# Optimization experiments

Measured on AMD Instinct MI355X. Metric: run time of the kernel, lower is better.

Reference implementation:

```python
import jax, jax.numpy as jnp
import numpy as np

BEV_H, BEV_W, ED, HEADS, HD, LEVELS, POINTS, LAYERS = 200, 200, 128, 8, 16, 4, 8, 2
SPATIAL = [(128, 256), (64, 128), (32, 64), (16, 32)]
NV = sum(h * w for h, w in SPATIAL)
NQ = BEV_H * BEV_W
NCLS = 21


def setup_inputs() -> dict:
    key = jax.random.key(0)
    ks = iter(jax.random.split(key, 48))
    r = lambda shape, s=0.02: jax.random.normal(next(ks), shape, jnp.float32) * s
    inp = dict(
        value=r((1, NV, ED), 1.0),
        bev_queries=r((NQ, ED), 0.02),
        bev_pos=r((NQ, ED), 0.02),
        proj_indices=jax.random.randint(next(ks), (1, BEV_H, BEV_W), 0, 250000),
        Wv=r((LAYERS, ED, ED)), bv=jnp.zeros((LAYERS, ED)),
        Woff=r((LAYERS, ED, HEADS * LEVELS * POINTS * 2), 0.01),
        boff=jnp.zeros((LAYERS, HEADS * LEVELS * POINTS * 2)),
        Wattn=r((LAYERS, ED, HEADS * LEVELS * POINTS), 0.01),
        battn=jnp.zeros((LAYERS, HEADS * LEVELS * POINTS)),
        Wout=r((LAYERS, ED, ED)), bout=jnp.zeros((LAYERS, ED)),
        Wf1=r((LAYERS, ED, ED)), bf1=jnp.zeros((LAYERS, ED)),
        Wf2=r((LAYERS, ED, ED)), bf2=jnp.zeros((LAYERS, ED)),
        ln_g=jnp.ones((LAYERS, 2, ED)), ln_b=jnp.zeros((LAYERS, 2, ED)),
        cw1=r((128, ED, 7, 7), 0.01), g1=jnp.ones(128), b1=jnp.zeros(128),
        cw2=r((64, 128, 3, 3), 0.02), g2=jnp.ones(64), b2=jnp.zeros(64),
        cw3=r((48, 64, 3, 3), 0.02), g3=jnp.ones(48), b3=jnp.zeros(48),
        cw4=r((48, 48, 3, 3), 0.02), g4=jnp.ones(48), b4=jnp.zeros(48),
        objw=r((NCLS, 48, 1, 1), 0.05), objb=jnp.zeros(NCLS),
    )
    return inp


def _ln(x, g, b):
    m = x.mean(-1, keepdims=True)
    v = ((x - m) ** 2).mean(-1, keepdims=True)
    return (x - m) * jax.lax.rsqrt(v + 1e-5) * g + b


def _deform_attn(q, value, Wv, bv, Woff, boff, Wattn, battn, Wout, bout, ref):
    # multi-scale deformable attention (Deformable-DETR / BEVFormer core)
    v = (value[0] @ Wv + bv).reshape(NV, HEADS, HD)
    off = (q @ Woff + boff).reshape(NQ, HEADS, LEVELS, POINTS, 2)
    attn = jax.nn.softmax((q @ Wattn + battn).reshape(NQ, HEADS, LEVELS * POINTS), -1)
    attn = attn.reshape(NQ, HEADS, LEVELS, POINTS)
    out = jnp.zeros((HEADS, NQ, HD), jnp.float32)
    start = 0
    for l, (H, W) in enumerate(SPATIAL):
        vl = v[start:start + H * W].transpose(1, 0, 2)  # [HEADS, H*W, HD]
        start += H * W
        # normalized sampling locations in [0,1]
        loc = ref[:, None, None, :] + off[:, :, l] / jnp.array([W, H], jnp.float32)
        x = loc[..., 0] * W - 0.5  # grid_sample align_corners=False convention
        y = loc[..., 1] * H - 0.5  # [NQ, HEADS, POINTS]
        x0 = jnp.floor(x)
        y0 = jnp.floor(y)
        acc = jnp.zeros((HEADS, NQ, POINTS, HD), jnp.float32)
        for dx, dy in ((0, 0), (1, 0), (0, 1), (1, 1)):
            xc = x0 + dx
            yc = y0 + dy
            wgt = (1.0 - jnp.abs(x - xc)) * (1.0 - jnp.abs(y - yc))
            valid = (xc >= 0) & (xc < W) & (yc >= 0) & (yc < H)
            xi = jnp.clip(xc, 0, W - 1).astype(jnp.int32)
            yi = jnp.clip(yc, 0, H - 1).astype(jnp.int32)
            idx = (yi * W + xi).transpose(1, 0, 2)  # [HEADS, NQ, POINTS]
            g = jax.vmap(lambda vh, ih: vh[ih])(vl, idx)  # [HEADS, NQ, POINTS, HD]
            acc = acc + (wgt * valid).transpose(1, 0, 2)[..., None] * g
        out = out + jnp.einsum('nhp,hnpd->hnd', attn[:, :, l], acc)
    return out.transpose(1, 0, 2).reshape(NQ, ED) @ Wout + bout


def _bev_encoder(bev_queries, bev_pos, value, Wv, bv, Woff, boff, Wattn, battn, Wout, bout, Wf1, bf1, Wf2, bf2, ln_g, ln_b):
    gx = (jnp.arange(BEV_W, dtype=jnp.float32) + 0.5) / BEV_W
    gy = (jnp.arange(BEV_H, dtype=jnp.float32) + 0.5) / BEV_H
    ref = jnp.stack(jnp.meshgrid(gx, gy), -1).reshape(NQ, 2)  # (x, y)
    q = bev_queries
    for i in range(LAYERS):  # operation_order: cross_attn, norm, ffn, norm
        a = _deform_attn(q + bev_pos, value, Wv[i], bv[i], Woff[i], boff[i],
                         Wattn[i], battn[i], Wout[i], bout[i], ref)
        q = _ln(q + a, ln_g[i, 0], ln_b[i, 0])
        h = jax.nn.relu(q @ Wf1[i] + bf1[i]) @ Wf2[i] + bf2[i]
        q = _ln(q + h, ln_g[i, 1], ln_b[i, 1])
    return q


def _conv(x, w, p):
    return jax.lax.conv_general_dilated(x, w, (1, 1), [(p, p), (p, p)],
                                        dimension_numbers=('NCHW', 'OIHW', 'NCHW'))


def _bn_relu(x, g, b):
    m = x.mean((0, 2, 3), keepdims=True)
    v = x.var((0, 2, 3), keepdims=True)
    return jax.nn.relu((x - m) * jax.lax.rsqrt(v + 1e-5) * g[None, :, None, None] + b[None, :, None, None])


def reference(value, bev_queries, bev_pos, proj_indices, Wv, bv, Woff, boff, Wattn, battn, Wout, bout, Wf1, bf1, Wf2, bf2, ln_g, ln_b, cw1, g1, b1, cw2, g2, b2, cw3, g3, b3, cw4, g4, b4, objw, objb):
    observed_masks = proj_indices < jnp.max(proj_indices)  # mask_update
    q = _bev_encoder(bev_queries, bev_pos, value, Wv, bv, Woff, boff, Wattn, battn,
                     Wout, bout, Wf1, bf1, Wf2, bf2, ln_g, ln_b)
    mem = q.reshape(1, BEV_H, BEV_W, ED).transpose(0, 3, 1, 2)  # [1, ED, H, W]
    h = _bn_relu(_conv(mem, cw1, 3), g1, b1)
    h = _bn_relu(_conv(h, cw2, 1), g2, b2)
    h = _bn_relu(_conv(h, cw3, 1), g3, b3)
    h = _bn_relu(_conv(h, cw4, 1), g4, b4)
    semmap = _conv(h, objw, 0) + objb[None, :, None, None]
    return semmap, observed_masks
```

## Files before the change

### kernel.cpp

```cpp
#include <hip/hip_runtime.h>
#include <cstdint>
#include <cstddef>

#define NQ 40000
#define EDIM 128
#define NVAL 43520
#define NCLS 21

typedef unsigned short u16;
typedef unsigned int uint;
typedef short bf16x8 __attribute__((ext_vector_type(8)));
typedef float f32x4 __attribute__((ext_vector_type(4)));

__device__ inline u16 f2b(float f) {
    unsigned u = __float_as_uint(f);
    unsigned r = u + 0x7FFF + ((u >> 16) & 1);
    return (u16)(r >> 16);
}
__device__ inline float b2f(u16 v) {
    unsigned u = ((unsigned)v) << 16;
    return __uint_as_float(u);
}
__device__ inline float blo(uint u) { return __uint_as_float(u << 16); }
__device__ inline float bhi(uint u) { return __uint_as_float(u & 0xFFFF0000u); }

__global__ void reduce_max_int(const int* __restrict__ idx, int* __restrict__ mx) {
    int i = blockIdx.x * 256 + threadIdx.x;
    int v = (i < NQ) ? idx[i] : 0;
    for (int o = 32; o > 0; o >>= 1) v = max(v, __shfl_xor(v, o, 64));
    if ((threadIdx.x & 63) == 0) atomicMax(mx, v);
}

__global__ void write_mask(const int* __restrict__ idx, const int* __restrict__ mx,
                           float* __restrict__ out) {
    int i = blockIdx.x * 256 + threadIdx.x;
    if (i >= NQ) return;
    out[i] = (idx[i] < *mx) ? 1.0f : 0.0f;
}

__global__ void cvt_b_k(const float* __restrict__ src, u16* __restrict__ dst, int n8) {
    int i = blockIdx.x * 256 + threadIdx.x;
    if (i >= n8) return;
    const float4 a = ((const float4*)src)[i * 2];
    const float4 b = ((const float4*)src)[i * 2 + 1];
    u16 o[8] = {f2b(a.x), f2b(a.y), f2b(a.z), f2b(a.w), f2b(b.x), f2b(b.y), f2b(b.z), f2b(b.w)};
    ((uint4*)dst)[i] = *(const uint4*)o;
}

__global__ void add2b_k(const float* __restrict__ a, const float* __restrict__ b,
                        u16* __restrict__ c, int n8) {
    int i = blockIdx.x * 256 + threadIdx.x;
    if (i >= n8) return;
    const float4 a0 = ((const float4*)a)[i * 2], a1 = ((const float4*)a)[i * 2 + 1];
    const float4 b0 = ((const float4*)b)[i * 2], b1 = ((const float4*)b)[i * 2 + 1];
    u16 o[8] = {f2b(a0.x + b0.x), f2b(a0.y + b0.y), f2b(a0.z + b0.z), f2b(a0.w + b0.w),
                f2b(a1.x + b1.x), f2b(a1.y + b1.y), f2b(a1.z + b1.z), f2b(a1.w + b1.w)};
    ((uint4*)c)[i] = *(const uint4*)o;
}

__global__ void pack_enc_k(const float* __restrict__ Wv, const float* __restrict__ Woff,
                           const float* __restrict__ Wattn, const float* __restrict__ Wout,
                           const float* __restrict__ Wf1, const float* __restrict__ Wf2,
                           u16* __restrict__ dst) {
    int i = blockIdx.x * 256 + threadIdx.x;
    if (i >= 327680) return;
    int l = i / 163840, r = i % 163840;
    int k = r / 1280, col = r % 1280;
    const float* src; int N; int n; u16* d;
    u16* base = dst + (size_t)l * 163840;
    if (col < 128)       { src = Wv    + (size_t)l * 16384; N = 128; n = col;        d = base;          }
    else if (col < 640)  { src = Woff  + (size_t)l * 65536; N = 512; n = col - 128;  d = base + 16384;  }
    else if (col < 896)  { src = Wattn + (size_t)l * 32768; N = 256; n = col - 640;  d = base + 81920;  }
    else if (col < 1024) { src = Wout  + (size_t)l * 16384; N = 128; n = col - 896;  d = base + 114688; }
    else if (col < 1152) { src = Wf1   + (size_t)l * 16384; N = 128; n = col - 1024; d = base + 131072; }
    else                 { src = Wf2   + (size_t)l * 16384; N = 128; n = col - 1152; d = base + 147456; }
    d[(size_t)n * 128 + k] = f2b(src[(size_t)k * N + n]);
}

__global__ void pack_bias_k(const float* __restrict__ boff, const float* __restrict__ battn,
                            float* __restrict__ dst) {
    int i = blockIdx.x * 256 + threadIdx.x;
    if (i >= 1536) return;
    int l = i / 768, r = i % 768;
    dst[i] = (r < 512) ? boff[(size_t)l * 512 + r] : battn[(size_t)l * 256 + r - 512];
}

__global__ void pack_cw_k(const float* __restrict__ w, u16* __restrict__ wT,
                          int OC, int IC, int KS, int OCp, int ICp) {
    int i = blockIdx.x * 256 + threadIdx.x;
    int tot = KS * KS * OCp * ICp;
    if (i >= tot) return;
    int ic = i % ICp; int r = i / ICp;
    int oc = r % OCp; int tap = r / OCp;
    int ky = tap / KS, kx = tap % KS;
    float v = 0.f;
    if (oc < OC && ic < IC)
        v = w[(((size_t)oc * IC + ic) * KS + ky) * KS + kx];
    wT[i] = f2b(v);
}

__global__ __launch_bounds__(256) void gemm_mfma_k(
        const u16* __restrict__ A, const u16* __restrict__ BT,
        const float* __restrict__ bias, float* __restrict__ Cf,
        u16* __restrict__ Cb, int N, int relu) {
    __shared__ u16 As[64 * 136];
    __shared__ u16 Bs[64 * 136];
    const int m0 = blockIdx.x * 64, n0 = blockIdx.y * 64;
    const int t = threadIdx.x;
#pragma unroll
    for (int ci = t; ci < 1024; ci += 256) {
        int r = ci >> 4, c = ci & 15;
        *(uint4*)&As[r * 136 + c * 8] = *(const uint4*)&A[(size_t)(m0 + r) * 128 + c * 8];
        *(uint4*)&Bs[r * 136 + c * 8] = *(const uint4*)&BT[(size_t)(n0 + r) * 128 + c * 8];
    }
    __syncthreads();
    const int wave = t >> 6, lane = t & 63;
    const int wm = (wave & 1) * 32, wn = (wave >> 1) * 32;
    const int lr = lane & 15, lk = (lane >> 4) * 8;
    f32x4 acc[2][2] = {};
#pragma unroll
    for (int ks = 0; ks < 4; ks++) {
        bf16x8 a0 = *(const bf16x8*)&As[(wm + lr) * 136 + ks * 32 + lk];
        bf16x8 a1 = *(const bf16x8*)&As[(wm + 16 + lr) * 136 + ks * 32 + lk];
        bf16x8 b0 = *(const bf16x8*)&Bs[(wn + lr) * 136 + ks * 32 + lk];
        bf16x8 b1 = *(const bf16x8*)&Bs[(wn + 16 + lr) * 136 + ks * 32 + lk];
        acc[0][0] = __builtin_amdgcn_mfma_f32_16x16x32_bf16(a0, b0, acc[0][0], 0, 0, 0);
        acc[0][1] = __builtin_amdgcn_mfma_f32_16x16x32_bf16(a0, b1, acc[0][1], 0, 0, 0);
        acc[1][0] = __builtin_amdgcn_mfma_f32_16x16x32_bf16(a1, b0, acc[1][0], 0, 0, 0);
        acc[1][1] = __builtin_amdgcn_mfma_f32_16x16x32_bf16(a1, b1, acc[1][1], 0, 0, 0);
    }
    float bj0 = bias[n0 + wn + lr];
    float bj1 = bias[n0 + wn + 16 + lr];
#pragma unroll
    for (int i = 0; i < 2; i++) {
#pragma unroll
        for (int j = 0; j < 2; j++) {
            float bb = j ? bj1 : bj0;
#pragma unroll
            for (int r = 0; r < 4; r++) {
                int ml = wm + i * 16 + (lane >> 4) * 4 + r;
                int nl = wn + j * 16 + lr;
                float v = acc[i][j][r] + bb;
                if (relu) v = fmaxf(v, 0.f);
                size_t o = (size_t)(m0 + ml) * N + n0 + nl;
                if (Cf) Cf[o] = v;
                if (Cb) Cb[o] = f2b(v);
            }
        }
    }
}

template <int KS, int ICP>
__global__ __launch_bounds__(256) void conv5_mfma_k(
        const u16* __restrict__ pimg, const u16* __restrict__ wT,
        float* __restrict__ out, int OCtot) {
    constexpr int PAD = KS / 2;
    constexpr int WIN = 64 + KS - 1;
    constexpr int STR = ICP + 8;
    constexpr int KSTEPS = ICP / 32;
    constexpr int NTAP = KS * KS;
    constexpr int ACH = WIN * (ICP / 8);
    constexpr int NB = ICP / 32;
    __shared__ u16 As[2 * WIN * STR];
    __shared__ u16 Bs[2 * 64 * STR];
    const int bx = blockIdx.x;
    const int yp = (bx >> 2) * 2;
    const int xc = bx & 3;
    const int x0 = (xc == 3) ? 136 : xc * 64;
    const int n0 = blockIdx.y * 64;
    const int t = threadIdx.x;
    const int wave = t >> 6, lane = t & 63;
    const int row = wave >> 1;
    const int wn = (wave & 1) * 32;
    const int lr = lane & 15, lkq = lane >> 4, lk = lkq * 8;

    f32x4 acc[4][2] = {};
    const u16* wbase = wT + (size_t)n0 * ICP;

    uint4 breg[NB];
    int bro[NB], bco[NB];
#pragma unroll
    for (int k = 0; k < NB; k++) {
        int ci = t + k * 256;
        bro[k] = ci / (ICP / 8);
        bco[k] = ci - bro[k] * (ICP / 8);
    }
#pragma unroll
    for (int k = 0; k < NB; k++)
        breg[k] = *(const uint4*)&wbase[(size_t)bro[k] * ICP + bco[k] * 8];
#pragma unroll
    for (int k = 0; k < NB; k++)
        *(uint4*)&Bs[(size_t)bro[k] * STR + bco[k] * 8] = breg[k];

    for (int ky = 0; ky < KS; ky++) {
        __syncthreads();
        {
            const u16* s0 = pimg + (((size_t)(yp + ky + 3 - PAD)) * 208 + (x0 + 3 - PAD)) * ICP;
            const u16* s1 = pimg + (((size_t)(yp + 1 + ky + 3 - PAD)) * 208 + (x0 + 3 - PAD)) * ICP;
            for (int ci = t; ci < 2 * ACH; ci += 256) {
                int w2 = ci / ACH, rem = ci - w2 * ACH;
                int r = rem / (ICP / 8), c = rem - r * (ICP / 8);
                const u16* s = w2 ? s1 : s0;
                *(uint4*)&As[(size_t)(w2 * WIN + r) * STR + c * 8] =
                    *(const uint4*)&s[(size_t)r * ICP + c * 8];
            }
        }
        for (int kx = 0; kx < KS; kx++) {
            const int tap = ky * KS + kx;
            __syncthreads();
            if (tap + 1 < NTAP) {
                const u16* ws = wbase + (size_t)(tap + 1) * OCtot * ICP;
#pragma unroll
                for (int k = 0; k < NB; k++)
                    breg[k] = *(const uint4*)&ws[(size_t)bro[k] * ICP + bco[k] * 8];
            }
            const u16* ab = &As[((size_t)row * WIN + kx) * STR];
            const u16* bb = &Bs[(size_t)((tap & 1) * 64 + wn) * STR];
#pragma unroll
            for (int ks = 0; ks < KSTEPS; ks++) {
                bf16x8 b0 = *(const bf16x8*)&bb[(size_t)lr * STR + ks * 32 + lk];
                bf16x8 b1 = *(const bf16x8*)&bb[(size_t)(lr + 16) * STR + ks * 32 + lk];
#pragma unroll
                for (int i = 0; i < 4; i++) {
                    bf16x8 a = *(const bf16x8*)&ab[(size_t)(lr + i * 16) * STR + ks * 32 + lk];
                    acc[i][0] = __builtin_amdgcn_mfma_f32_16x16x32_bf16(a, b0, acc[i][0], 0, 0, 0);
                    acc[i][1] = __builtin_amdgcn_mfma_f32_16x16x32_bf16(a, b1, acc[i][1], 0, 0, 0);
                }
            }
            if (tap + 1 < NTAP) {
                u16* bd = &Bs[(size_t)(((tap + 1) & 1) * 64) * STR];
#pragma unroll
                for (int k = 0; k < NB; k++)
                    *(uint4*)&bd[(size_t)bro[k] * STR + bco[k] * 8] = breg[k];
            }
        }
    }
    const int px0 = (yp + row) * 200 + x0;
#pragma unroll
    for (int i = 0; i < 4; i++) {
#pragma unroll
        for (int j = 0; j < 2; j++) {
#pragma unroll
            for (int r = 0; r < 4; r++) {
                int ml = i * 16 + lkq * 4 + r;
                int nl = wn + j * 16 + lr;
                out[(size_t)(px0 + ml) * OCtot + n0 + nl] = acc[i][j][r];
            }
        }
    }
}

__global__ __launch_bounds__(256) void deform3_k(
        const u16* __restrict__ v, const u16* __restrict__ oa,
        u16* __restrict__ outb, int q0, int nq) {
    const int t = threadIdx.x;
    const int wq = t >> 6;
    const int lane = t & 63;
    const int s = lane >> 5;
    const int l32 = lane & 31;
    const int h = l32 >> 2;
    const int cl = l32 & 3;
    const int qi = blockIdx.x * 8 + wq * 2 + s;
    if (qi >= nq) return;
    const int gq = q0 + qi;
    const float rx = ((gq % 200) + 0.5f) / 200.f;
    const float ry = ((gq / 200) + 0.5f) / 200.f;

    const uint* lp = (const uint*)(oa + (size_t)qi * 768 + 512 + h * 32);
    float lg[32];
#pragma unroll
    for (int i = 0; i < 16; i++) { uint u = lp[i]; lg[2 * i] = blo(u); lg[2 * i + 1] = bhi(u); }
    float mx = -1e30f;
#pragma unroll
    for (int i = 0; i < 32; i++) mx = fmaxf(mx, lg[i]);
    float ssum = 0.f;
#pragma unroll
    for (int i = 0; i < 32; i++) { lg[i] = __expf(lg[i] - mx); ssum += lg[i]; }
    const float inv = 1.f / ssum;

    const uint* op = (const uint*)(oa + (size_t)qi * 768 + h * 64);

    const int HS[4] = {128, 64, 32, 16};
    const int WS[4] = {256, 128, 64, 32};
    const int ST[4] = {0, 32768, 40960, 43008};
    float a0 = 0.f, a1 = 0.f, a2 = 0.f, a3 = 0.f;
#pragma unroll
    for (int l = 0; l < 4; l++) {
        const int H = HS[l], W = WS[l];
        const float fW = (float)W, fH = (float)H;
        const u16* vb = v + (size_t)ST[l] * 128 + h * 16 + cl * 4;
#pragma unroll
        for (int p = 0; p < 8; p++) {
            uint pr = op[l * 8 + p];
            float ox = blo(pr), oy = bhi(pr);
            float xx = rx * fW + ox - 0.5f;
            float yy = ry * fH + oy - 0.5f;
            float xf = floorf(xx), yf = floorf(yy);
            int ix = (int)xf, iy = (int)yf;
            float fx = xx - xf, fy = yy - yf;
            float aw = lg[l * 8 + p] * inv;
            int x1 = ix + 1, y1 = iy + 1;
            bool vx0 = (unsigned)ix < (unsigned)W;
            bool vx1 = (unsigned)x1 < (unsigned)W;
            bool vy0 = (unsigned)iy < (unsigned)H;
            bool vy1 = (unsigned)y1 < (unsigned)H;
            int cx0 = min(max(ix, 0), W - 1), cx1 = min(max(x1, 0), W - 1);
            int cy0 = min(max(iy, 0), H - 1), cy1 = min(max(y1, 0), H - 1);
            float w00 = (vx0 && vy0) ? (1.f - fx) * (1.f - fy) * aw : 0.f;
            float w10 = (vx1 && vy0) ? fx * (1.f - fy) * aw : 0.f;
            float w01 = (vx0 && vy1) ? (1.f - fx) * fy * aw : 0.f;
            float w11 = (vx1 && vy1) ? fx * fy * aw : 0.f;
            uint2 u00 = *(const uint2*)(vb + (size_t)(cy0 * W + cx0) * 128);
            uint2 u10 = *(const uint2*)(vb + (size_t)(cy0 * W + cx1) * 128);
            uint2 u01 = *(const uint2*)(vb + (size_t)(cy1 * W + cx0) * 128);
            uint2 u11 = *(const uint2*)(vb + (size_t)(cy1 * W + cx1) * 128);
            a0 = fmaf(w00, blo(u00.x), a0); a1 = fmaf(w00, bhi(u00.x), a1);
            a2 = fmaf(w00, blo(u00.y), a2); a3 = fmaf(w00, bhi(u00.y), a3);
            a0 = fmaf(w10, blo(u10.x), a0); a1 = fmaf(w10, bhi(u10.x), a1);
            a2 = fmaf(w10, blo(u10.y), a2); a3 = fmaf(w10, bhi(u10.y), a3);
            a0 = fmaf(w01, blo(u01.x), a0); a1 = fmaf(w01, bhi(u01.x), a1);
            a2 = fmaf(w01, blo(u01.y), a2); a3 = fmaf(w01, bhi(u01.y), a3);
            a0 = fmaf(w11, blo(u11.x), a0); a1 = fmaf(w11, bhi(u11.x), a1);
            a2 = fmaf(w11, blo(u11.y), a2); a3 = fmaf(w11, bhi(u11.y), a3);
        }
    }
    uint2 o;
    o.x = (uint)f2b(a0) | ((uint)f2b(a1) << 16);
    o.y = (uint)f2b(a2) | ((uint)f2b(a3) << 16);
    *(uint2*)(outb + (size_t)gq * 128 + h * 16 + cl * 4) = o;
}

__global__ __launch_bounds__(256) void add_ln_k(
        float* __restrict__ q, const float* __restrict__ a,
        const float* __restrict__ g, const float* __restrict__ b,
        u16* __restrict__ qb) {
    const int row = blockIdx.x * 4 + (threadIdx.x >> 6);
    const int lane = threadIdx.x & 63;
    float s0 = q[(size_t)row * 128 + lane] + a[(size_t)row * 128 + lane];
    float s1 = q[(size_t)row * 128 + 64 + lane] + a[(size_t)row * 128 + 64 + lane];
    float sum = s0 + s1;
    for (int o = 32; o > 0; o >>= 1) sum += __shfl_xor(sum, o, 64);
    float mean = sum * (1.f / 128.f);
    float d0 = s0 - mean, d1 = s1 - mean;
    float vs = d0 * d0 + d1 * d1;
    for (int o = 32; o > 0; o >>= 1) vs += __shfl_xor(vs, o, 64);
    float inv = rsqrtf(vs * (1.f / 128.f) + 1e-5f);
    float o0 = d0 * inv * g[lane] + b[lane];
    float o1 = d1 * inv * g[64 + lane] + b[64 + lane];
    q[(size_t)row * 128 + lane] = o0;
    q[(size_t)row * 128 + 64 + lane] = o1;
    qb[(size_t)row * 128 + lane] = f2b(o0);
    qb[(size_t)row * 128 + 64 + lane] = f2b(o1);
}

__global__ void fill_pimg2_k(const u16* __restrict__ qb, u16* __restrict__ pimg) {
    int i = blockIdx.x * 256 + threadIdx.x;
    if (i >= 685568) return;
    int pp = i >> 4, c8 = i & 15;
    int py = pp / 208, px = pp - py * 208;
    uint4 val = {0u, 0u, 0u, 0u};
    if (py >= 3 && py < 203 && px >= 3 && px < 203)
        val = ((const uint4*)qb)[((size_t)((py - 3) * 200 + (px - 3))) * 16 + c8];
    ((uint4*)pimg)[i] = val;
}

__global__ __launch_bounds__(256) void bn_stats2_k(const float* __restrict__ x,
                                                   float* __restrict__ acc,
                                                   int cSh, int ppb) {
    const int t = threadIdx.x;
    const int Cp = 1 << cSh;
    const int c = t & (Cp - 1);
    const int sub = t >> cSh;
    const int nsub = 256 >> cSh;
    float s = 0.f, s2 = 0.f;
    const int pbase = blockIdx.x * ppb;
    for (int i = sub; i < ppb; i += nsub) {
        float v = x[(size_t)(pbase + i) * Cp + c];
        s += v; s2 += v * v;
    }
    __shared__ float ls[256], ls2[256];
    ls[t] = s; ls2[t] = s2;
    __syncthreads();
    if (t < Cp) {
        for (int k = 1; k < nsub; k++) { s += ls[t + k * Cp]; s2 += ls2[t + k * Cp]; }
        atomicAdd(&acc[2 * t], s);
        atomicAdd(&acc[2 * t + 1], s2);
    }
}

__global__ void bn_fin_k(const float* __restrict__ acc, float* __restrict__ mv, int C) {
    int t = threadIdx.x;
    if (t >= C) return;
    float m = acc[2 * t] * (1.f / 40000.f);
    float var = acc[2 * t + 1] * (1.f / 40000.f) - m * m;
    mv[2 * t] = m;
    mv[2 * t + 1] = rsqrtf(var + 1e-5f);
}

__global__ void bn_apply_pad2_k(const float* __restrict__ x, const float* __restrict__ mv,
                                const float* __restrict__ g, const float* __restrict__ b,
                                u16* __restrict__ outp, int cSh, int Creal) {
    int i = blockIdx.x * 256 + threadIdx.x;
    int Cp = 1 << cSh;
    if (i >= 206 * 208 * Cp) return;
    int c = i & (Cp - 1);
    int pp = i >> cSh;
    int py = pp / 208, px = pp - py * 208;
    float v = 0.f;
    if (c < Creal && py >= 3 && py < 203 && px >= 3 && px < 203) {
        int p = (py - 3) * 200 + (px - 3);
        v = fmaxf((x[(size_t)p * Cp + c] - mv[2 * c]) * mv[2 * c + 1] * g[c] + b[c], 0.f);
    }
    outp[i] = f2b(v);
}

__global__ void bn_apply2_k(const float* __restrict__ x, const float* __restrict__ mv,
                            const float* __restrict__ g, const float* __restrict__ b,
                            u16* __restrict__ outb, int cSh, int Creal) {
    int i = blockIdx.x * 256 + threadIdx.x;
    int Cp = 1 << cSh;
    if (i >= 40000 * Cp) return;
    int c = i & (Cp - 1);
    float v = 0.f;
    if (c < Creal) v = fmaxf((x[i] - mv[2 * c]) * mv[2 * c + 1] * g[c] + b[c], 0.f);
    outb[i] = f2b(v);
}

__global__ void obj_conv_k(const u16* __restrict__ in, const float* __restrict__ w,
                           const float* __restrict__ bias, float* __restrict__ out) {
    int p = blockIdx.x * 256 + threadIdx.x;
    if (p >= 40000) return;
    float xin[48];
#pragma unroll
    for (int c = 0; c < 48; c++) xin[c] = b2f(in[(size_t)p * 64 + c]);
    for (int o = 0; o < NCLS; o++) {
        float acc = bias[o];
#pragma unroll
        for (int c = 0; c < 48; c++) acc += xin[c] * w[o * 48 + c];
        out[(size_t)o * 40000 + p] = acc;
    }
}

extern "C" void kernel_launch(void* const* d_in, const int* in_sizes, int n_in,
                              void* d_out, int out_size, void* d_ws, size_t ws_size,
                              hipStream_t stream) {
    const float* value   = (const float*)d_in[0];
    const float* bev_q   = (const float*)d_in[1];
    const float* bev_pos = (const float*)d_in[2];
    const int*   proj    = (const int*)d_in[3];
    const float* Wv      = (const float*)d_in[4];
    const float* bv      = (const float*)d_in[5];
    const float* Woff    = (const float*)d_in[6];
    const float* boff    = (const float*)d_in[7];
    const float* Wattn   = (const float*)d_in[8];
    const float* battn   = (const float*)d_in[9];
    const float* Wout    = (const float*)d_in[10];
    const float* bout    = (const float*)d_in[11];
    const float* Wf1     = (const float*)d_in[12];
    const float* bf1     = (const float*)d_in[13];
    const float* Wf2     = (const float*)d_in[14];
    const float* bf2     = (const float*)d_in[15];
    const float* ln_g    = (const float*)d_in[16];
    const float* ln_b    = (const float*)d_in[17];
    const float* cw1     = (const float*)d_in[18];
    const float* g1      = (const float*)d_in[19];
    const float* b1      = (const float*)d_in[20];
    const float* cw2     = (const float*)d_in[21];
    const float* g2      = (const float*)d_in[22];
    const float* b2      = (const float*)d_in[23];
    const float* cw3     = (const float*)d_in[24];
    const float* g3      = (const float*)d_in[25];
    const float* b3      = (const float*)d_in[26];
    const float* cw4     = (const float*)d_in[27];
    const float* g4      = (const float*)d_in[28];
    const float* b4      = (const float*)d_in[29];
    const float* objw    = (const float*)d_in[30];
    const float* objb    = (const float*)d_in[31];
    float* out = (float*)d_out;

    float* WSb = (float*)d_ws;
    float* q     = WSb + 0;
    u16*   qb    = (u16*)(WSb + 5120000);
    u16*   qpb   = (u16*)(WSb + 7680000);
    u16*   valb  = (u16*)(WSb + 10240000);
    u16*   vbufb = (u16*)(WSb + 13025280);
    u16*   fb    = (u16*)(WSb + 15810560);
    float* tmp   = WSb + 18882560;
    u16*   aob   = (u16*)(WSb + 24002560);
    u16*   hb    = (u16*)(WSb + 26562560);
    u16*   wenc  = (u16*)(WSb + 29122560);
    u16*   wcv   = (u16*)(WSb + 29286400);
    float* bnacc = WSb + 29761536;
    float* bnmv  = WSb + 29762048;
    int*   maxi  = (int*)(WSb + 29762304);
    float* fbias = WSb + 29762308;

    u16*   pimg = (u16*)(WSb + 10240000);
    float* c1f  = tmp;
    u16*   c1b  = (u16*)(WSb + 13025280);
    float* c2f  = WSb + 0;
    u16*   c2b  = (u16*)(WSb + 5120000);
    float* c3f  = WSb + 2560000;
    u16*   c3b  = (u16*)(WSb + 7680000);
    float* c4f  = WSb + 0;
    u16*   c4b  = (u16*)(WSb + 15810560);

    const size_t L = 163840;
    u16* WvT[2]; u16* WoffT[2]; u16* WoutT[2]; u16* Wf1T[2]; u16* Wf2T[2];
    for (int l = 0; l < 2; l++) {
        u16* base = wenc + l * L;
        WvT[l]    = base;
        WoffT[l]  = base + 16384;
        WoutT[l]  = base + 114688;
        Wf1T[l]   = base + 131072;
        Wf2T[l]   = base + 147456;
    }
    u16* w1T = wcv;
    u16* w2T = wcv + 802816;
    u16* w3T = wcv + 876544;
    u16* w4T = wcv + 913408;

    hipMemsetAsync(maxi, 0, sizeof(int), stream);
    reduce_max_int<<<157, 256, 0, stream>>>(proj, maxi);
    write_mask<<<157, 256, 0, stream>>>(proj, maxi, out + 840000);

    pack_enc_k<<<1280, 256, 0, stream>>>(Wv, Woff, Wattn, Wout, Wf1, Wf2, wenc);
    pack_bias_k<<<6, 256, 0, stream>>>(boff, battn, fbias);
    pack_cw_k<<<3136, 256, 0, stream>>>(cw1, w1T, 128, 128, 7, 128, 128);
    pack_cw_k<<<288, 256, 0, stream>>>(cw2, w2T, 64, 128, 3, 64, 128);
    pack_cw_k<<<144, 256, 0, stream>>>(cw3, w3T, 48, 64, 3, 64, 64);
    pack_cw_k<<<144, 256, 0, stream>>>(cw4, w4T, 48, 48, 3, 64, 64);
    cvt_b_k<<<2720, 256, 0, stream>>>(value, valb, NVAL * 128 / 8);

    hipMemcpyAsync(q, bev_q, (size_t)NQ * EDIM * sizeof(float),
                   hipMemcpyDeviceToDevice, stream);
    const int CH0 = 19968, CH1 = 20032;
    for (int l = 0; l < 2; l++) {
        gemm_mfma_k<<<dim3(680, 2), 256, 0, stream>>>(
            valb, WvT[l], bv + (size_t)l * 128, nullptr, vbufb, 128, 0);
        add2b_k<<<2500, 256, 0, stream>>>(q, bev_pos, qpb, NQ * 128 / 8);
        for (int cidx = 0; cidx < 2; cidx++) {
            int qs = cidx ? CH0 : 0;
            int nq = cidx ? CH1 : CH0;
            gemm_mfma_k<<<dim3(nq / 64, 12), 256, 0, stream>>>(
                qpb + (size_t)qs * 128, WoffT[l], fbias + (size_t)l * 768,
                nullptr, fb, 768, 0);
            deform3_k<<<nq / 8, 256, 0, stream>>>(vbufb, fb, aob, qs, nq);
        }
        gemm_mfma_k<<<dim3(625, 2), 256, 0, stream>>>(
            aob, WoutT[l], bout + (size_t)l * 128, tmp, nullptr, 128, 0);
        add_ln_k<<<10000, 256, 0, stream>>>(q, tmp, ln_g + (size_t)(l * 2 + 0) * 128,
                                            ln_b + (size_t)(l * 2 + 0) * 128, qb);
        gemm_mfma_k<<<dim3(625, 2), 256, 0, stream>>>(
            qb, Wf1T[l], bf1 + (size_t)l * 128, nullptr, hb, 128, 1);
        gemm_mfma_k<<<dim3(625, 2), 256, 0, stream>>>(
            hb, Wf2T[l], bf2 + (size_t)l * 128, tmp, nullptr, 128, 0);
        add_ln_k<<<10000, 256, 0, stream>>>(q, tmp, ln_g + (size_t)(l * 2 + 1) * 128,
                                            ln_b + (size_t)(l * 2 + 1) * 128, qb);
    }

    fill_pimg2_k<<<2678, 256, 0, stream>>>(qb, pimg);

    conv5_mfma_k<7, 128><<<dim3(400, 2), 256, 0, stream>>>(pimg, w1T, c1f, 128);
    hipMemsetAsync(bnacc, 0, 512 * sizeof(float), stream);
    bn_stats2_k<<<125, 256, 0, stream>>>(c1f, bnacc, 7, 320);
    bn_fin_k<<<1, 128, 0, stream>>>(bnacc, bnmv, 128);
    bn_apply_pad2_k<<<21424, 256, 0, stream>>>(c1f, bnmv, g1, b1, c1b, 7, 128);

    conv5_mfma_k<3, 128><<<dim3(400, 1), 256, 0, stream>>>(c1b, w2T, c2f, 64);
    hipMemsetAsync(bnacc, 0, 512 * sizeof(float), stream);
    bn_stats2_k<<<125, 256, 0, stream>>>(c2f, bnacc, 6, 320);
    bn_fin_k<<<1, 64, 0, stream>>>(bnacc, bnmv, 64);
    bn_apply_pad2_k<<<10712, 256, 0, stream>>>(c2f, bnmv, g2, b2, c2b, 6, 64);

    conv5_mfma_k<3, 64><<<dim3(400, 1), 256, 0, stream>>>(c2b, w3T, c3f, 64);
    hipMemsetAsync(bnacc, 0, 512 * sizeof(float), stream);
    bn_stats2_k<<<125, 256, 0, stream>>>(c3f, bnacc, 6, 320);
    bn_fin_k<<<1, 48, 0, stream>>>(bnacc, bnmv, 48);
    bn_apply_pad2_k<<<10712, 256, 0, stream>>>(c3f, bnmv, g3, b3, c3b, 6, 48);

    conv5_mfma_k<3, 64><<<dim3(400, 1), 256, 0, stream>>>(c3b, w4T, c4f, 64);
    hipMemsetAsync(bnacc, 0, 512 * sizeof(float), stream);
    bn_stats2_k<<<125, 256, 0, stream>>>(c4f, bnacc, 6, 320);
    bn_fin_k<<<1, 48, 0, stream>>>(bnacc, bnmv, 48);
    bn_apply2_k<<<10000, 256, 0, stream>>>(c4f, bnmv, g4, b4, c4b, 6, 48);

    obj_conv_k<<<157, 256, 0, stream>>>(c4b, objw, objb, out);
}
```

Baseline: 1.024 ms.

## Fuse BN stats into conv epilogue, reuse A tile across N, widen deform gathers

BatchNorm sum and sum-of-squares are now accumulated in the conv epilogue through wave shuffles and atomics, which removes the separate bn_stats pass that re-read each conv output. Duplicated edge pixels in the last x-chunk are masked out. The GEMM kernel now loops over several 64-wide N subtiles per block and loads the A tile once, so the activation matrix is read fewer times, at the cost of fewer blocks. The deformable attention kernel has each lane gather 8 channels with 16-byte loads and handle 4 queries per wave instead of 2, which cuts load instruction count but raises register use per lane.

Measured after the change: 3.899 ms. 281% more time.

```diff
diff --git a/kernel.cpp b/kernel.cpp
--- a/kernel.cpp
+++ b/kernel.cpp
@@ -99,52 +99,58 @@
     wT[i] = f2b(v);
 }
 
-__global__ __launch_bounds__(256) void gemm_mfma_k(
+__global__ __launch_bounds__(256) void gemm2_mfma_k(
         const u16* __restrict__ A, const u16* __restrict__ BT,
         const float* __restrict__ bias, float* __restrict__ Cf,
-        u16* __restrict__ Cb, int N, int relu) {
+        u16* __restrict__ Cb, int N, int relu, int NSUB) {
     __shared__ u16 As[64 * 136];
     __shared__ u16 Bs[64 * 136];
-    const int m0 = blockIdx.x * 64, n0 = blockIdx.y * 64;
+    const int m0 = blockIdx.x * 64;
+    const int nbase = blockIdx.y * 64 * NSUB;
     const int t = threadIdx.x;
-#pragma unroll
-    for (int ci = t; ci < 1024; ci += 256) {
-        int r = ci >> 4, c = ci & 15;
-        *(uint4*)&As[r * 136 + c * 8] = *(const uint4*)&A[(size_t)(m0 + r) * 128 + c * 8];
-        *(uint4*)&Bs[r * 136 + c * 8] = *(const uint4*)&BT[(size_t)(n0 + r) * 128 + c * 8];
-    }
-    __syncthreads();
     const int wave = t >> 6, lane = t & 63;
     const int wm = (wave & 1) * 32, wn = (wave >> 1) * 32;
-    const int lr = lane & 15, lk = (lane >> 4) * 8;
-    f32x4 acc[2][2] = {};
-#pragma unroll
-    for (int ks = 0; ks < 4; ks++) {
-        bf16x8 a0 = *(const bf16x8*)&As[(wm + lr) * 136 + ks * 32 + lk];
-        bf16x8 a1 = *(const bf16x8*)&As[(wm + 16 + lr) * 136 + ks * 32 + lk];
-        bf16x8 b0 = *(const bf16x8*)&Bs[(wn + lr) * 136 + ks * 32 + lk];
-        bf16x8 b1 = *(const bf16x8*)&Bs[(wn + 16 + lr) * 136 + ks * 32 + lk];
-        acc[0][0] = __builtin_amdgcn_mfma_f32_16x16x32_bf16(a0, b0, acc[0][0], 0, 0, 0);
-        acc[0][1] = __builtin_amdgcn_mfma_f32_16x16x32_bf16(a0, b1, acc[0][1], 0, 0, 0);
-        acc[1][0] = __builtin_amdgcn_mfma_f32_16x16x32_bf16(a1, b0, acc[1][0], 0, 0, 0);
-        acc[1][1] = __builtin_amdgcn_mfma_f32_16x16x32_bf16(a1, b1, acc[1][1], 0, 0, 0);
-    }
-    float bj0 = bias[n0 + wn + lr];
-    float bj1 = bias[n0 + wn + 16 + lr];
-#pragma unroll
-    for (int i = 0; i < 2; i++) {
-#pragma unroll
-        for (int j = 0; j < 2; j++) {
-            float bb = j ? bj1 : bj0;
-#pragma unroll
-            for (int r = 0; r < 4; r++) {
-                int ml = wm + i * 16 + (lane >> 4) * 4 + r;
-                int nl = wn + j * 16 + lr;
-                float v = acc[i][j][r] + bb;
-                if (relu) v = fmaxf(v, 0.f);
-                size_t o = (size_t)(m0 + ml) * N + n0 + nl;
-                if (Cf) Cf[o] = v;
-                if (Cb) Cb[o] = f2b(v);
+    const int lr = lane & 15, lkq = lane >> 4, lk = lkq * 8;
+    for (int s = 0; s < NSUB; s++) {
+        const int n0 = nbase + s * 64;
+        if (s) __syncthreads();
+#pragma unroll
+        for (int ci = t; ci < 1024; ci += 256) {
+            int r = ci >> 4, c = (ci & 15) * 8;
+            if (s == 0)
+                *(uint4*)&As[r * 136 + c] = *(const uint4*)&A[(size_t)(m0 + r) * 128 + c];
+            *(uint4*)&Bs[r * 136 + c] = *(const uint4*)&BT[(size_t)(n0 + r) * 128 + c];
+        }
+        __syncthreads();
+        f32x4 acc[2][2] = {};
+#pragma unroll
+        for (int ks = 0; ks < 4; ks++) {
+            bf16x8 a0 = *(const bf16x8*)&As[(wm + lr) * 136 + ks * 32 + lk];
+            bf16x8 a1 = *(const bf16x8*)&As[(wm + 16 + lr) * 136 + ks * 32 + lk];
+            bf16x8 b0 = *(const bf16x8*)&Bs[(wn + lr) * 136 + ks * 32 + lk];
+            bf16x8 b1 = *(const bf16x8*)&Bs[(wn + 16 + lr) * 136 + ks * 32 + lk];
+            acc[0][0] = __builtin_amdgcn_mfma_f32_16x16x32_bf16(a0, b0, acc[0][0], 0, 0, 0);
+            acc[0][1] = __builtin_amdgcn_mfma_f32_16x16x32_bf16(a0, b1, acc[0][1], 0, 0, 0);
+            acc[1][0] = __builtin_amdgcn_mfma_f32_16x16x32_bf16(a1, b0, acc[1][0], 0, 0, 0);
+            acc[1][1] = __builtin_amdgcn_mfma_f32_16x16x32_bf16(a1, b1, acc[1][1], 0, 0, 0);
+        }
+        float bj0 = bias[n0 + wn + lr];
+        float bj1 = bias[n0 + wn + 16 + lr];
+#pragma unroll
+        for (int i = 0; i < 2; i++) {
+#pragma unroll
+            for (int j = 0; j < 2; j++) {
+                float bb = j ? bj1 : bj0;
+#pragma unroll
+                for (int r = 0; r < 4; r++) {
+                    int ml = wm + i * 16 + lkq * 4 + r;
+                    int nl = wn + j * 16 + lr;
+                    float v = acc[i][j][r] + bb;
+                    if (relu) v = fmaxf(v, 0.f);
+                    size_t o = (size_t)(m0 + ml) * N + n0 + nl;
+                    if (Cf) Cf[o] = v;
+                    if (Cb) Cb[o] = f2b(v);
+                }
             }
         }
     }
@@ -153,7 +159,7 @@
 template <int KS, int ICP>
 __global__ __launch_bounds__(256) void conv5_mfma_k(
         const u16* __restrict__ pimg, const u16* __restrict__ wT,
-        float* __restrict__ out, int OCtot) {
+        float* __restrict__ out, float* __restrict__ bnacc, int OCtot) {
     constexpr int PAD = KS / 2;
     constexpr int WIN = 64 + KS - 1;
     constexpr int STR = ICP + 8;
@@ -183,14 +189,14 @@
     for (int k = 0; k < NB; k++) {
         int ci = t + k * 256;
         bro[k] = ci / (ICP / 8);
-        bco[k] = ci - bro[k] * (ICP / 8);
+        bco[k] = (ci % (ICP / 8)) * 8;
     }
 #pragma unroll
     for (int k = 0; k < NB; k++)
-        breg[k] = *(const uint4*)&wbase[(size_t)bro[k] * ICP + bco[k] * 8];
+        breg[k] = *(const uint4*)&wbase[(size_t)bro[k] * ICP + bco[k]];
 #pragma unroll
     for (int k = 0; k < NB; k++)
-        *(uint4*)&Bs[(size_t)bro[k] * STR + bco[k] * 8] = breg[k];
+        *(uint4*)&Bs[bro[k] * STR + bco[k]] = breg[k];
 
     for (int ky = 0; ky < KS; ky++) {
         __syncthreads();
@@ -212,7 +218,7 @@
                 const u16* ws = wbase + (size_t)(tap + 1) * OCtot * ICP;
 #pragma unroll
                 for (int k = 0; k < NB; k++)
-                    breg[k] = *(const uint4*)&ws[(size_t)bro[k] * ICP + bco[k] * 8];
+                    breg[k] = *(const uint4*)&ws[(size_t)bro[k] * ICP + bco[k]];
             }
             const u16* ab = &As[((size_t)row * WIN + kx) * STR];
             const u16* bb = &Bs[(size_t)((tap & 1) * 64 + wn) * STR];
@@ -231,36 +237,47 @@
                 u16* bd = &Bs[(size_t)(((tap + 1) & 1) * 64) * STR];
 #pragma unroll
                 for (int k = 0; k < NB; k++)
-                    *(uint4*)&bd[(size_t)bro[k] * STR + bco[k] * 8] = breg[k];
+                    *(uint4*)&bd[bro[k] * STR + bco[k]] = breg[k];
             }
         }
     }
     const int px0 = (yp + row) * 200 + x0;
 #pragma unroll
-    for (int i = 0; i < 4; i++) {
-#pragma unroll
-        for (int j = 0; j < 2; j++) {
+    for (int j = 0; j < 2; j++) {
+        float sa = 0.f, sb = 0.f;
+#pragma unroll
+        for (int i = 0; i < 4; i++) {
 #pragma unroll
             for (int r = 0; r < 4; r++) {
                 int ml = i * 16 + lkq * 4 + r;
                 int nl = wn + j * 16 + lr;
-                out[(size_t)(px0 + ml) * OCtot + n0 + nl] = acc[i][j][r];
-            }
-        }
-    }
-}
-
-__global__ __launch_bounds__(256) void deform3_k(
+                float v = acc[i][j][r];
+                out[(size_t)(px0 + ml) * OCtot + n0 + nl] = v;
+                float msk = (xc != 3 || ml >= 56) ? 1.f : 0.f;
+                sa += msk * v;
+                sb += msk * v * v;
+            }
+        }
+        sa += __shfl_xor(sa, 16, 64); sb += __shfl_xor(sb, 16, 64);
+        sa += __shfl_xor(sa, 32, 64); sb += __shfl_xor(sb, 32, 64);
+        if (lkq == 0) {
+            int ch = n0 + wn + j * 16 + lr;
+            atomicAdd(&bnacc[2 * ch], sa);
+            atomicAdd(&bnacc[2 * ch + 1], sb);
+        }
+    }
+}
+
+__global__ __launch_bounds__(256) void deform5_k(
         const u16* __restrict__ v, const u16* __restrict__ oa,
         u16* __restrict__ outb, int q0, int nq) {
     const int t = threadIdx.x;
     const int wq = t >> 6;
     const int lane = t & 63;
-    const int s = lane >> 5;
-    const int l32 = lane & 31;
-    const int h = l32 >> 2;
-    const int cl = l32 & 3;
-    const int qi = blockIdx.x * 8 + wq * 2 + s;
+    const int qs = lane >> 4;
+    const int h = (lane >> 1) & 7;
+    const int oct = lane & 1;
+    const int qi = blockIdx.x * 16 + wq * 4 + qs;
     if (qi >= nq) return;
     const int gq = q0 + qi;
     const float rx = ((gq % 200) + 0.5f) / 200.f;
@@ -283,12 +300,12 @@
     const int HS[4] = {128, 64, 32, 16};
     const int WS[4] = {256, 128, 64, 32};
     const int ST[4] = {0, 32768, 40960, 43008};
-    float a0 = 0.f, a1 = 0.f, a2 = 0.f, a3 = 0.f;
+    float acc[8] = {};
 #pragma unroll
     for (int l = 0; l < 4; l++) {
         const int H = HS[l], W = WS[l];
         const float fW = (float)W, fH = (float)H;
-        const u16* vb = v + (size_t)ST[l] * 128 + h * 16 + cl * 4;
+        const u16* vb = v + (size_t)ST[l] * 128 + h * 16 + oct * 8;
 #pragma unroll
         for (int p = 0; p < 8; p++) {
             uint pr = op[l * 8 + p];
@@ -310,24 +327,31 @@
             float w10 = (vx1 && vy0) ? fx * (1.f - fy) * aw : 0.f;
             float w01 = (vx0 && vy1) ? (1.f - fx) * fy * aw : 0.f;
             float w11 = (vx1 && vy1) ? fx * fy * aw : 0.f;
-            uint2 u00 = *(const uint2*)(vb + (size_t)(cy0 * W + cx0) * 128);
-            uint2 u10 = *(const uint2*)(vb + (size_t)(cy0 * W + cx1) * 128);
-            uint2 u01 = *(const uint2*)(vb + (size_t)(cy1 * W + cx0) * 128);
-            uint2 u11 = *(const uint2*)(vb + (size_t)(cy1 * W + cx1) * 128);
-            a0 = fmaf(w00, blo(u00.x), a0); a1 = fmaf(w00, bhi(u00.x), a1);
-            a2 = fmaf(w00, blo(u00.y), a2); a3 = fmaf(w00, bhi(u00.y), a3);
-            a0 = fmaf(w10, blo(u10.x), a0); a1 = fmaf(w10, bhi(u10.x), a1);
-            a2 = fmaf(w10, blo(u10.y), a2); a3 = fmaf(w10, bhi(u10.y), a3);
-            a0 = fmaf(w01, blo(u01.x), a0); a1 = fmaf(w01, bhi(u01.x), a1);
-            a2 = fmaf(w01, blo(u01.y), a2); a3 = fmaf(w01, bhi(u01.y), a3);
-            a0 = fmaf(w11, blo(u11.x), a0); a1 = fmaf(w11, bhi(u11.x), a1);
-            a2 = fmaf(w11, blo(u11.y), a2); a3 = fmaf(w11, bhi(u11.y), a3);
-        }
-    }
-    uint2 o;
-    o.x = (uint)f2b(a0) | ((uint)f2b(a1) << 16);
-    o.y = (uint)f2b(a2) | ((uint)f2b(a3) << 16);
-    *(uint2*)(outb + (size_t)gq * 128 + h * 16 + cl * 4) = o;
+            uint4 u00 = *(const uint4*)(vb + (size_t)(cy0 * W + cx0) * 128);
+            uint4 u10 = *(const uint4*)(vb + (size_t)(cy0 * W + cx1) * 128);
+            uint4 u01 = *(const uint4*)(vb + (size_t)(cy1 * W + cx0) * 128);
+            uint4 u11 = *(const uint4*)(vb + (size_t)(cy1 * W + cx1) * 128);
+            const uint a00[4] = {u00.x, u00.y, u00.z, u00.w};
+            const uint a10[4] = {u10.x, u10.y, u10.z, u10.w};
+            const uint a01[4] = {u01.x, u01.y, u01.z, u01.w};
+            const uint a11[4] = {u11.x, u11.y, u11.z, u11.w};
+#pragma unroll
+            for (int c = 0; c < 4; c++) {
+                acc[2 * c]     = fmaf(w00, blo(a00[c]), acc[2 * c]);
+                acc[2 * c + 1] = fmaf(w00, bhi(a00[c]), acc[2 * c + 1]);
+                acc[2 * c]     = fmaf(w10, blo(a10[c]), acc[2 * c]);
+                acc[2 * c + 1] = fmaf(w10, bhi(a10[c]), acc[2 * c + 1]);
+                acc[2 * c]     = fmaf(w01, blo(a01[c]), acc[2 * c]);
+                acc[2 * c + 1] = fmaf(w01, bhi(a01[c]), acc[2 * c + 1]);
+                acc[2 * c]     = fmaf(w11, blo(a11[c]), acc[2 * c]);
+                acc[2 * c + 1] = fmaf(w11, bhi(a11[c]), acc[2 * c + 1]);
+            }
+        }
+    }
+    u16 o[8];
+#pragma unroll
+    for (int c = 0; c < 8; c++) o[c] = f2b(acc[c]);
+    *(uint4*)(outb + (size_t)gq * 128 + h * 16 + oct * 8) = *(const uint4*)o;
 }
 
 __global__ __launch_bounds__(256) void add_ln_k(
@@ -362,30 +386,6 @@
     if (py >= 3 && py < 203 && px >= 3 && px < 203)
         val = ((const uint4*)qb)[((size_t)((py - 3) * 200 + (px - 3))) * 16 + c8];
     ((uint4*)pimg)[i] = val;
-}
-
-__global__ __launch_bounds__(256) void bn_stats2_k(const float* __restrict__ x,
-                                                   float* __restrict__ acc,
-                                                   int cSh, int ppb) {
-    const int t = threadIdx.x;
-    const int Cp = 1 << cSh;
-    const int c = t & (Cp - 1);
-    const int sub = t >> cSh;
-    const int nsub = 256 >> cSh;
-    float s = 0.f, s2 = 0.f;
-    const int pbase = blockIdx.x * ppb;
-    for (int i = sub; i < ppb; i += nsub) {
-        float v = x[(size_t)(pbase + i) * Cp + c];
-        s += v; s2 += v * v;
-    }
-    __shared__ float ls[256], ls2[256];
-    ls[t] = s; ls2[t] = s2;
-    __syncthreads();
-    if (t < Cp) {
-        for (int k = 1; k < nsub; k++) { s += ls[t + k * Cp]; s2 += ls2[t + k * Cp]; }
-        atomicAdd(&acc[2 * t], s);
-        atomicAdd(&acc[2 * t + 1], s2);
-    }
 }
 
 __global__ void bn_fin_k(const float* __restrict__ acc, float* __restrict__ mv, int C) {
@@ -536,52 +536,48 @@
                    hipMemcpyDeviceToDevice, stream);
     const int CH0 = 19968, CH1 = 20032;
     for (int l = 0; l < 2; l++) {
-        gemm_mfma_k<<<dim3(680, 2), 256, 0, stream>>>(
-            valb, WvT[l], bv + (size_t)l * 128, nullptr, vbufb, 128, 0);
+        gemm2_mfma_k<<<dim3(680, 1), 256, 0, stream>>>(
+            valb, WvT[l], bv + (size_t)l * 128, nullptr, vbufb, 128, 0, 2);
         add2b_k<<<2500, 256, 0, stream>>>(q, bev_pos, qpb, NQ * 128 / 8);
         for (int cidx = 0; cidx < 2; cidx++) {
             int qs = cidx ? CH0 : 0;
             int nq = cidx ? CH1 : CH0;
-            gemm_mfma_k<<<dim3(nq / 64, 12), 256, 0, stream>>>(
+            gemm2_mfma_k<<<dim3(nq / 64, 3), 256, 0, stream>>>(
                 qpb + (size_t)qs * 128, WoffT[l], fbias + (size_t)l * 768,
-                nullptr, fb, 768, 0);
-            deform3_k<<<nq / 8, 256, 0, stream>>>(vbufb, fb, aob, qs, nq);
-        }
-        gemm_mfma_k<<<dim3(625, 2), 256, 0, stream>>>(
-            aob, WoutT[l], bout + (size_t)l * 128, tmp, nullptr, 128, 0);
+                nullptr, fb, 768, 0, 4);
+            deform5_k<<<nq / 16, 256, 0, stream>>>(vbufb, fb, aob, qs, nq);
+        }
+        gemm2_mfma_k<<<dim3(625, 1), 256, 0, stream>>>(
+            aob, WoutT[l], bout + (size_t)l * 128, tmp, nullptr, 128, 0, 2);
         add_ln_k<<<10000, 256, 0, stream>>>(q, tmp, ln_g + (size_t)(l * 2 + 0) * 128,
                                             ln_b + (size_t)(l * 2 + 0) * 128, qb);
-        gemm_mfma_k<<<dim3(625, 2), 256, 0, stream>>>(
-            qb, Wf1T[l], bf1 + (size_t)l * 128, nullptr, hb, 128, 1);
-        gemm_mfma_k<<<dim3(625, 2), 256, 0, stream>>>(
-            hb, Wf2T[l], bf2 + (size_t)l * 128, tmp, nullptr, 128, 0);
+        gemm2_mfma_k<<<dim3(625, 1), 256, 0, stream>>>(
+            qb, Wf1T[l], bf1 + (size_t)l * 128, nullptr, hb, 128, 1, 2);
+        gemm2_mfma_k<<<dim3(625, 1), 256, 0, stream>>>(
+            hb, Wf2T[l], bf2 + (size_t)l * 128, tmp, nullptr, 128, 0, 2);
         add_ln_k<<<10000, 256, 0, stream>>>(q, tmp, ln_g + (size_t)(l * 2 + 1) * 128,
                                             ln_b + (size_t)(l * 2 + 1) * 128, qb);
     }
 
     fill_pimg2_k<<<2678, 256, 0, stream>>>(qb, pimg);
 
-    conv5_mfma_k<7, 128><<<dim3(400, 2), 256, 0, stream>>>(pimg, w1T, c1f, 128);
     hipMemsetAsync(bnacc, 0, 512 * sizeof(float), stream);
-    bn_stats2_k<<<125, 256, 0, stream>>>(c1f, bnacc, 7, 320);
+    conv5_mfma_k<7, 128><<<dim3(400, 2), 256, 0, stream>>>(pimg, w1T, c1f, bnacc, 128);
     bn_fin_k<<<1, 128, 0, stream>>>(bnacc, bnmv, 128);
     bn_apply_pad2_k<<<21424, 256, 0, stream>>>(c1f, bnmv, g1, b1, c1b, 7, 128);
 
-    conv5_mfma_k<3, 128><<<dim3(400, 1), 256, 0, stream>>>(c1b, w2T, c2f, 64);
     hipMemsetAsync(bnacc, 0, 512 * sizeof(float), stream);
-    bn_stats2_k<<<125, 256, 0, stream>>>(c2f, bnacc, 6, 320);
+    conv5_mfma_k<3, 128><<<dim3(400, 1), 256, 0, stream>>>(c1b, w2T, c2f, bnacc, 64);
     bn_fin_k<<<1, 64, 0, stream>>>(bnacc, bnmv, 64);
     bn_apply_pad2_k<<<10712, 256, 0, stream>>>(c2f, bnmv, g2, b2, c2b, 6, 64);
 
-    conv5_mfma_k<3, 64><<<dim3(400, 1), 256, 0, stream>>>(c2b, w3T, c3f, 64);
     hipMemsetAsync(bnacc, 0, 512 * sizeof(float), stream);
-    bn_stats2_k<<<125, 256, 0, stream>>>(c3f, bnacc, 6, 320);
+    conv5_mfma_k<3, 64><<<dim3(400, 1), 256, 0, stream>>>(c2b, w3T, c3f, bnacc, 64);
     bn_fin_k<<<1, 48, 0, stream>>>(bnacc, bnmv, 48);
     bn_apply_pad2_k<<<10712, 256, 0, stream>>>(c3f, bnmv, g3, b3, c3b, 6, 48);
 
-    conv5_mfma_k<3, 64><<<dim3(400, 1), 256, 0, stream>>>(c3b, w4T, c4f, 64);
     hipMemsetAsync(bnacc, 0, 512 * sizeof(float), stream);
-    bn_stats2_k<<<125, 256, 0, stream>>>(c4f, bnacc, 6, 320);
+    conv5_mfma_k<3, 64><<<dim3(400, 1), 256, 0, stream>>>(c3b, w4T, c4f, bnacc, 64);
     bn_fin_k<<<1, 48, 0, stream>>>(bnacc, bnmv, 48);
     bn_apply2_k<<<10000, 256, 0, stream>>>(c4f, bnmv, g4, b4, c4b, 6, 48);
 
```
